# Optimization experiments

Hardware: AMD Instinct MI355X
Metric: run time of the kernel (lower is better)

The kernel has to match this reference:

```python
import jax, jax.numpy as jnp
import numpy as np

N = 100000
E = 1000000
F_IN = 128
HID = 64
HEADS = 4
NC = 4


def setup_inputs() -> dict:
    key = jax.random.key(0)
    ks = jax.random.split(key, 24)
    s = 0.05
    inp = {
        "x": jax.random.normal(ks[0], (N, F_IN), jnp.float32),
        "edge_index": jax.random.randint(ks[1], (2, E), 0, N, jnp.int64 if jax.config.jax_enable_x64 else jnp.int32),
        "edge_weight": jax.random.uniform(ks[2], (E,), jnp.float32),
        "node_mask": jnp.ones((N,), jnp.bool_),
        # GCNConv: lin (no bias applied pre-propagate in math below; bias added after)
        "gcn_W": s * jax.random.normal(ks[3], (F_IN, HID), jnp.float32),
        "gcn_b": jnp.zeros((HID,), jnp.float32),
        "proj_W": s * jax.random.normal(ks[4], (F_IN, HID), jnp.float32),
        "proj_b": jnp.zeros((HID,), jnp.float32),
        "ln1_g": jnp.ones((HID,), jnp.float32), "ln1_b": jnp.zeros((HID,), jnp.float32),
        # GATv2Conv heads=4, concat=False: lin_l, lin_r -> [F, H*C], att [H, C], bias [C]
        "gat_Wl": s * jax.random.normal(ks[5], (HID, HEADS * HID), jnp.float32),
        "gat_Wr": s * jax.random.normal(ks[6], (HID, HEADS * HID), jnp.float32),
        "gat_att": s * jax.random.normal(ks[7], (HEADS, HID), jnp.float32),
        "gat_b": jnp.zeros((HID,), jnp.float32),
        "ln2_g": jnp.ones((HID,), jnp.float32), "ln2_b": jnp.zeros((HID,), jnp.float32),
        # SAGEConv: lin_l (neighbors, with bias), lin_r (root, no bias)
        "sage_Wl": s * jax.random.normal(ks[8], (HID, HID), jnp.float32),
        "sage_bl": jnp.zeros((HID,), jnp.float32),
        "sage_Wr": s * jax.random.normal(ks[9], (HID, HID), jnp.float32),
        "ln3_g": jnp.ones((HID,), jnp.float32), "ln3_b": jnp.zeros((HID,), jnp.float32),
        # edge MLP: Linear(2*HID+1, 32) -> ReLU -> Linear(32, 1)
        "emlp_W1": s * jax.random.normal(ks[10], (2 * HID + 1, 32), jnp.float32),
        "emlp_b1": jnp.zeros((32,), jnp.float32),
        "emlp_W2": s * jax.random.normal(ks[11], (32, 1), jnp.float32),
        "emlp_b2": jnp.zeros((1,), jnp.float32),
        # heads on JK-cat dim 3*HID
        "mort_W": s * jax.random.normal(ks[12], (3 * HID, 1), jnp.float32),
        "mort_b": jnp.zeros((1,), jnp.float32),
        "hours_W": s * jax.random.normal(ks[13], (3 * HID, 1), jnp.float32),
        "hours_b": jnp.zeros((1,), jnp.float32),
        "disc_W": s * jax.random.normal(ks[14], (3 * HID, NC), jnp.float32),
        "disc_b": jnp.zeros((NC,), jnp.float32),
    }
    return inp


def _ln(h, g, b, eps=1e-5):
    mu = jnp.mean(h, axis=-1, keepdims=True)
    var = jnp.mean(jnp.square(h - mu), axis=-1, keepdims=True)
    return (h - mu) * jax.lax.rsqrt(var + eps) * g + b


def reference(x, edge_index, edge_weight, node_mask,
              gcn_W, gcn_b, proj_W, proj_b, ln1_g, ln1_b,
              gat_Wl, gat_Wr, gat_att, gat_b, ln2_g, ln2_b,
              sage_Wl, sage_bl, sage_Wr, ln3_g, ln3_b,
              emlp_W1, emlp_b1, emlp_W2, emlp_b2,
              mort_W, mort_b, hours_W, hours_b, disc_W, disc_b):
    n = x.shape[0]
    src, dst = edge_index[0], edge_index[1]
    loop = jnp.arange(n, dtype=src.dtype)
    s2 = jnp.concatenate([src, loop])  # edges + self loops (GCN, GATv2)
    d2 = jnp.concatenate([dst, loop])

    # ---- GCNConv (normalized, self loops with weight 1) ----
    w2 = jnp.concatenate([edge_weight, jnp.ones((n,), x.dtype)])
    deg = jax.ops.segment_sum(w2, d2, num_segments=n)
    dinv = jnp.where(deg > 0, jax.lax.rsqrt(deg), 0.0)
    norm = dinv[s2] * w2 * dinv[d2]
    xw = x @ gcn_W  # [N, HID]
    gcn_out = jax.ops.segment_sum(norm[:, None] * xw[s2], d2, num_segments=n) + gcn_b
    h1 = jax.nn.relu(_ln(gcn_out, ln1_g, ln1_b))
    h_init = h1 + (x @ proj_W + proj_b)

    # ---- edge-gated edge MLP (recomputed weights; unused by later convs, kept for fidelity) ----
    feat = jnp.concatenate([h_init[src], h_init[dst], edge_weight[:, None]], axis=1)
    _new_ew = jax.nn.sigmoid((jax.nn.relu(feat @ emlp_W1 + emlp_b1) @ emlp_W2 + emlp_b2)[:, 0])

    # ---- GATv2Conv (heads=4, concat=False -> mean over heads, self loops) ----
    H, C = gat_att.shape
    xl = (h_init @ gat_Wl).reshape(n, H, C)
    xr = (h_init @ gat_Wr).reshape(n, H, C)
    e = jax.nn.leaky_relu(xl[s2] + xr[d2], 0.2)        # [E+N, H, C]
    score = jnp.einsum('ehc,hc->eh', e, gat_att)        # [E+N, H]
    smax = jax.ops.segment_max(score, d2, num_segments=n)
    ex = jnp.exp(score - smax[d2])
    den = jax.ops.segment_sum(ex, d2, num_segments=n)
    alpha = ex / den[d2]
    gat_out = jax.ops.segment_sum(alpha[:, :, None] * xl[s2], d2, num_segments=n)
    gat_out = jnp.mean(gat_out, axis=1) + gat_b
    h2 = jax.nn.relu(_ln(gat_out, ln2_g, ln2_b)) + h_init

    # ---- SAGEConv (mean aggregation, root weight, no self loops) ----
    nsum = jax.ops.segment_sum(h2[src], dst, num_segments=n)
    cnt = jax.ops.segment_sum(jnp.ones(src.shape, h2.dtype), dst, num_segments=n)
    nmean = nsum / jnp.maximum(cnt, 1.0)[:, None]
    sage_out = nmean @ sage_Wl + sage_bl + h2 @ sage_Wr
    h3 = jax.nn.relu(_ln(sage_out, ln3_g, ln3_b)) + h2

    # ---- JumpingKnowledge cat + masked readout + heads ----
    x_jk = jnp.concatenate([h_init, h2, h3], axis=1)  # [N, 3*HID]
    readout = jnp.where(node_mask[:, None], x_jk, 0.0)
    mort = (readout @ mort_W + mort_b)[:, 0]
    hours = (readout @ hours_W + hours_b)[:, 0]
    disc = readout @ disc_W + disc_b
    return mort, hours, disc
```

## Files before the change

kernel.cpp:

```cpp
#include <hip/hip_runtime.h>
#include <hip/hip_fp16.h>
#include <math.h>

#define N_NODES 100000
#define N_EDGES 1000000
#define F_IN    128
#define HID     64
#define HEADS   4
#define NCLS    4
#define SCAN_BLK 98
#define GEMM_NT 5

typedef _Float16 half8 __attribute__((ext_vector_type(8)));
typedef _Float16 fp16x2 __attribute__((ext_vector_type(2)));
typedef float f32x4 __attribute__((ext_vector_type(4)));

__device__ __forceinline__ float wsum(float v) {
#pragma unroll
  for (int o = 32; o > 0; o >>= 1) v += __shfl_xor(v, o, 64);
  return v;
}
struct Half4 { __half2 a, b; };
__device__ __forceinline__ __half2 absh2(__half2 v) {
  unsigned u; __builtin_memcpy(&u, &v, 4);
  u &= 0x7FFF7FFFu;
  __half2 r; __builtin_memcpy(&r, &u, 4);
  return r;
}
__device__ __forceinline__ float fdot2f(__half2 a, __half2 b, float c) {
#if defined(__has_builtin) && __has_builtin(__builtin_amdgcn_fdot2)
  fp16x2 av, bv;
  __builtin_memcpy(&av, &a, 4); __builtin_memcpy(&bv, &b, 4);
  return __builtin_amdgcn_fdot2(av, bv, c, false);
#else
  float2 af = __half22float2(a), bf = __half22float2(b);
  return c + af.x * bf.x + af.y * bf.y;
#endif
}
__device__ __forceinline__ float edge_score(Half4 A, __half2 Ra, __half2 Rb,
                                            __half2 at0, __half2 at1,
                                            __half2 c06, __half2 c04) {
  __half2 t0 = __hadd2(A.a, Ra), t1 = __hadd2(A.b, Rb);
  __half2 l0 = __hfma2(t0, c06, __hmul2(absh2(t0), c04));
  __half2 l1 = __hfma2(t1, c06, __hmul2(absh2(t1), c04));
  return fdot2f(l1, at1, fdot2f(l0, at0, 0.f));
}
__device__ __forceinline__ float reduce16(float q) {
  q += __shfl_xor(q, 1); q += __shfl_xor(q, 2);
  q += __shfl_xor(q, 4); q += __shfl_xor(q, 8);
  return q;
}
__device__ __forceinline__ int wave_node() {
  return __builtin_amdgcn_readfirstlane(blockIdx.x * 4 + (threadIdx.x >> 6));
}

__global__ void k_hist(const int* __restrict__ dst, int* __restrict__ cnt) {
  int e = blockIdx.x * 256 + threadIdx.x;
  if (e < N_EDGES) atomicAdd(&cnt[dst[e]], 1);
}
__global__ __launch_bounds__(256) void k_scan1(const int* __restrict__ cnt,
                                               int* __restrict__ partial,
                                               int* __restrict__ bsum) {
  __shared__ int lds[256];
  int t = threadIdx.x;
  int base = blockIdx.x * 1024 + t * 4;
  int v0 = (base + 0 < N_NODES) ? cnt[base + 0] : 0;
  int v1 = (base + 1 < N_NODES) ? cnt[base + 1] : 0;
  int v2 = (base + 2 < N_NODES) ? cnt[base + 2] : 0;
  int v3 = (base + 3 < N_NODES) ? cnt[base + 3] : 0;
  int s = v0 + v1 + v2 + v3;
  lds[t] = s;
  __syncthreads();
  for (int o = 1; o < 256; o <<= 1) {
    int x = (t >= o) ? lds[t - o] : 0;
    __syncthreads();
    lds[t] += x;
    __syncthreads();
  }
  int excl = lds[t] - s;
  if (base + 0 < N_NODES) partial[base + 0] = excl;
  if (base + 1 < N_NODES) partial[base + 1] = excl + v0;
  if (base + 2 < N_NODES) partial[base + 2] = excl + v0 + v1;
  if (base + 3 < N_NODES) partial[base + 3] = excl + v0 + v1 + v2;
  if (t == 255) bsum[blockIdx.x] = lds[255];
}
__global__ __launch_bounds__(256) void k_scan3(const int* __restrict__ partial,
                                               const int* __restrict__ bsum,
                                               int* __restrict__ row_ptr,
                                               int* __restrict__ cursor) {
  __shared__ int ex[128];
  int t = threadIdx.x;
  int orig = 0;
  if (t < 128) {
    orig = (t < SCAN_BLK) ? bsum[t] : 0;
    ex[t] = orig;
  }
  __syncthreads();
  for (int o = 1; o < 128; o <<= 1) {
    int x = (t < 128 && t >= o) ? ex[t - o] : 0;
    __syncthreads();
    if (t < 128) ex[t] += x;
    __syncthreads();
  }
  if (t < 128) ex[t] -= orig;
  __syncthreads();
  int i = blockIdx.x * 256 + t;
  if (i < N_NODES) {
    int v = partial[i] + ex[i >> 10];
    row_ptr[i] = v;
    cursor[i] = v;
  }
  if (i == 0) row_ptr[N_NODES] = N_EDGES;
}
__global__ void k_fill(const int* __restrict__ src, const int* __restrict__ dst,
                       const float* __restrict__ ew, int* __restrict__ cursor,
                       int* __restrict__ csr_src, float* __restrict__ csr_w) {
  int e = blockIdx.x * 256 + threadIdx.x;
  if (e >= N_EDGES) return;
  int d = dst[e];
  int p = atomicAdd(&cursor[d], 1);
  csr_src[p] = src[e];
  csr_w[p] = ew[e];
}

__global__ __launch_bounds__(512) void k_in_gemm_mfma(
    const float* __restrict__ x, const float* __restrict__ gcn_W,
    const float* __restrict__ proj_W, const float* __restrict__ proj_b,
    __half* __restrict__ xw16, __half* __restrict__ xp16) {
  __shared__ __half at[16 * 136];
  int t = threadIdx.x;
  int w = t >> 6, lane = t & 63;
  int m = lane & 15, q = lane >> 4;
  int ncol = w * 16 + m;
  const float* W = (ncol < 64) ? gcn_W : proj_W;
  int nc = (ncol < 64) ? ncol : ncol - 64;
  half8 bf[4];
#pragma unroll
  for (int ch = 0; ch < 4; ++ch) {
    int kb = ch * 32 + q * 8;
#pragma unroll
    for (int j = 0; j < 8; ++j)
      bf[ch][j] = (_Float16)W[(kb + j) * 64 + nc];
  }
  float pb = (ncol >= 64) ? proj_b[nc] : 0.f;
  int nb0 = blockIdx.x * (16 * GEMM_NT);
  for (int nt = 0; nt < GEMM_NT; ++nt) {
    int nb = nb0 + nt * 16;
    {
      int row = t >> 5, col = (t & 31) * 4;
      float4 v = *reinterpret_cast<const float4*>(x + (size_t)(nb + row) * F_IN + col);
      __half2* d = reinterpret_cast<__half2*>(&at[row * 136 + col]);
      d[0] = __floats2half2_rn(v.x, v.y);
      d[1] = __floats2half2_rn(v.z, v.w);
    }
    __syncthreads();
    f32x4 acc = {0.f, 0.f, 0.f, 0.f};
#pragma unroll
    for (int ch = 0; ch < 4; ++ch) {
      half8 af = *reinterpret_cast<const half8*>(&at[m * 136 + ch * 32 + q * 8]);
      acc = __builtin_amdgcn_mfma_f32_16x16x32_f16(af, bf[ch], acc, 0, 0, 0);
    }
    if (ncol < 64) {
#pragma unroll
      for (int r = 0; r < 4; ++r)
        xw16[(size_t)(nb + q * 4 + r) * HID + nc] = __float2half(acc[r]);
    } else {
#pragma unroll
      for (int r = 0; r < 4; ++r)
        xp16[(size_t)(nb + q * 4 + r) * HID + nc] = __float2half(acc[r] + pb);
    }
    __syncthreads();
  }
}

__global__ void k_deg(const int* __restrict__ row_ptr, const float* __restrict__ csr_w,
                      float* __restrict__ dinv) {
  int n = blockIdx.x * 256 + threadIdx.x;
  if (n >= N_NODES) return;
  float deg = 1.0f;
  int end = row_ptr[n + 1];
  for (int i = row_ptr[n]; i < end; ++i) deg += csr_w[i];
  dinv[n] = rsqrtf(deg);
}

__global__ __launch_bounds__(256) void k_gcn_fused(
    const int* __restrict__ row_ptr, const int* __restrict__ csr_src,
    const float* __restrict__ csr_w, const float* __restrict__ dinv,
    const __half* __restrict__ xw16, const __half* __restrict__ xp16,
    const float* __restrict__ gcn_b, const float* __restrict__ g,
    const float* __restrict__ bb, __half* __restrict__ h_init16) {
  int n = wave_node();
  int lane = threadIdx.x & 63;
  float di = dinv[n];
  float acc = di * di * __half2float(xw16[(size_t)n * HID + lane]);
  int beg = row_ptr[n], end = row_ptr[n + 1];
  int i = beg;
  for (; i + 4 <= end; i += 4) {
    int s0 = __builtin_amdgcn_readfirstlane(csr_src[i]);
    int s1 = __builtin_amdgcn_readfirstlane(csr_src[i + 1]);
    int s2 = __builtin_amdgcn_readfirstlane(csr_src[i + 2]);
    int s3 = __builtin_amdgcn_readfirstlane(csr_src[i + 3]);
    float nrm0 = dinv[s0] * csr_w[i] * di;
    float nrm1 = dinv[s1] * csr_w[i + 1] * di;
    float nrm2 = dinv[s2] * csr_w[i + 2] * di;
    float nrm3 = dinv[s3] * csr_w[i + 3] * di;
    float v0 = __half2float(xw16[(size_t)s0 * HID + lane]);
    float v1 = __half2float(xw16[(size_t)s1 * HID + lane]);
    float v2 = __half2float(xw16[(size_t)s2 * HID + lane]);
    float v3 = __half2float(xw16[(size_t)s3 * HID + lane]);
    acc += nrm0 * v0 + nrm1 * v1 + nrm2 * v2 + nrm3 * v3;
  }
  for (; i < end; ++i) {
    int s = __builtin_amdgcn_readfirstlane(csr_src[i]);
    float nrm = dinv[s] * csr_w[i] * di;
    acc += nrm * __half2float(xw16[(size_t)s * HID + lane]);
  }
  float v = acc + gcn_b[lane];
  float mu = wsum(v) * (1.f / HID);
  float dv = v - mu;
  float var = wsum(dv * dv) * (1.f / HID);
  float h = dv * rsqrtf(var + 1e-5f) * g[lane] + bb[lane];
  h = h > 0.f ? h : 0.f;
  h_init16[(size_t)n * HID + lane] =
      __float2half(h + __half2float(xp16[(size_t)n * HID + lane]));
}

__global__ __launch_bounds__(512) void k_gat_gemm_mfma(
    const __half* __restrict__ h16, const float* __restrict__ Wl,
    const float* __restrict__ Wr, __half* __restrict__ xl, __half* __restrict__ xr) {
  __shared__ __half at[16 * 72];
  int t = threadIdx.x;
  int w = t >> 6, lane = t & 63;
  int m = lane & 15, q = lane >> 4;
  half8 bf[4][2];
#pragma unroll
  for (int tt = 0; tt < 4; ++tt) {
    int c = w * 16 + tt * 128 + m;
    const float* W = (c < 256) ? Wl : Wr;
    int nc = (c < 256) ? c : c - 256;
#pragma unroll
    for (int ch = 0; ch < 2; ++ch) {
      int kb = ch * 32 + q * 8;
#pragma unroll
      for (int j = 0; j < 8; ++j)
        bf[tt][ch][j] = (_Float16)W[(kb + j) * 256 + nc];
    }
  }
  int nb0 = blockIdx.x * (16 * GEMM_NT);
  for (int nt = 0; nt < GEMM_NT; ++nt) {
    int nb = nb0 + nt * 16;
    {
      int row = t >> 5, col = (t & 31) * 2;
      *reinterpret_cast<__half2*>(&at[row * 72 + col]) =
          *reinterpret_cast<const __half2*>(h16 + (size_t)(nb + row) * HID + col);
    }
    __syncthreads();
    half8 a0 = *reinterpret_cast<const half8*>(&at[m * 72 + q * 8]);
    half8 a1 = *reinterpret_cast<const half8*>(&at[m * 72 + 32 + q * 8]);
#pragma unroll
    for (int tt = 0; tt < 4; ++tt) {
      f32x4 acc = {0.f, 0.f, 0.f, 0.f};
      acc = __builtin_amdgcn_mfma_f32_16x16x32_f16(a0, bf[tt][0], acc, 0, 0, 0);
      acc = __builtin_amdgcn_mfma_f32_16x16x32_f16(a1, bf[tt][1], acc, 0, 0, 0);
      int c = w * 16 + tt * 128 + m;
      __half* out = (c < 256) ? (xl + c) : (xr + (c - 256));
#pragma unroll
      for (int r = 0; r < 4; ++r)
        out[(size_t)(nb + q * 4 + r) * 256] = __float2half(acc[r]);
    }
    __syncthreads();
  }
}

__global__ __launch_bounds__(256) void k_gat_fused(
    const int* __restrict__ row_ptr, const int* __restrict__ csr_src,
    const __half* __restrict__ xl, const __half* __restrict__ xr,
    const float* __restrict__ att, const float* __restrict__ gat_b,
    const float* __restrict__ g, const float* __restrict__ bb,
    const __half* __restrict__ h_init16, __half* __restrict__ h2_16) {
  int n = wave_node();
  int lane = threadIdx.x & 63;
  const __half2 c06 = __float2half2_rn(0.6f);
  const __half2 c04 = __float2half2_rn(0.4f);
  float4 atv = *reinterpret_cast<const float4*>(att + lane * 4);
  __half2 at0 = __floats2half2_rn(atv.x, atv.y);
  __half2 at1 = __floats2half2_rn(atv.z, atv.w);
  Half4 R = *reinterpret_cast<const Half4*>(xr + (size_t)n * 256 + lane * 4);
  Half4 S = *reinterpret_cast<const Half4*>(xl + (size_t)n * 256 + lane * 4);

  float q = reduce16(edge_score(S, R.a, R.b, at0, at1, c06, c04));
  float w = __expf(q);
  float den = w;
  float2 f0 = __half22float2(S.a), f1 = __half22float2(S.b);
  float4 acc = make_float4(w * f0.x, w * f0.y, w * f1.x, w * f1.y);

  int beg = row_ptr[n], end = row_ptr[n + 1];
  int i = beg;
  for (; i + 4 <= end; i += 4) {
    int s0 = __builtin_amdgcn_readfirstlane(csr_src[i]);
    int s1 = __builtin_amdgcn_readfirstlane(csr_src[i + 1]);
    int s2 = __builtin_amdgcn_readfirstlane(csr_src[i + 2]);
    int s3 = __builtin_amdgcn_readfirstlane(csr_src[i + 3]);
    Half4 A0 = *reinterpret_cast<const Half4*>(xl + (size_t)s0 * 256 + lane * 4);
    Half4 A1 = *reinterpret_cast<const Half4*>(xl + (size_t)s1 * 256 + lane * 4);
    Half4 A2 = *reinterpret_cast<const Half4*>(xl + (size_t)s2 * 256 + lane * 4);
    Half4 A3 = *reinterpret_cast<const Half4*>(xl + (size_t)s3 * 256 + lane * 4);
    float q0 = edge_score(A0, R.a, R.b, at0, at1, c06, c04);
    float q1 = edge_score(A1, R.a, R.b, at0, at1, c06, c04);
    float q2 = edge_score(A2, R.a, R.b, at0, at1, c06, c04);
    float q3 = edge_score(A3, R.a, R.b, at0, at1, c06, c04);
    q0 += __shfl_xor(q0, 1); q1 += __shfl_xor(q1, 1);
    q2 += __shfl_xor(q2, 1); q3 += __shfl_xor(q3, 1);
    q0 += __shfl_xor(q0, 2); q1 += __shfl_xor(q1, 2);
    q2 += __shfl_xor(q2, 2); q3 += __shfl_xor(q3, 2);
    q0 += __shfl_xor(q0, 4); q1 += __shfl_xor(q1, 4);
    q2 += __shfl_xor(q2, 4); q3 += __shfl_xor(q3, 4);
    q0 += __shfl_xor(q0, 8); q1 += __shfl_xor(q1, 8);
    q2 += __shfl_xor(q2, 8); q3 += __shfl_xor(q3, 8);
    float w0 = __expf(q0), w1 = __expf(q1);
    float w2 = __expf(q2), w3 = __expf(q3);
    den += (w0 + w1) + (w2 + w3);
    float2 a00 = __half22float2(A0.a), a01 = __half22float2(A0.b);
    float2 a10 = __half22float2(A1.a), a11 = __half22float2(A1.b);
    float2 a20 = __half22float2(A2.a), a21 = __half22float2(A2.b);
    float2 a30 = __half22float2(A3.a), a31 = __half22float2(A3.b);
    acc.x += (w0 * a00.x + w1 * a10.x) + (w2 * a20.x + w3 * a30.x);
    acc.y += (w0 * a00.y + w1 * a10.y) + (w2 * a20.y + w3 * a30.y);
    acc.z += (w0 * a01.x + w1 * a11.x) + (w2 * a21.x + w3 * a31.x);
    acc.w += (w0 * a01.y + w1 * a11.y) + (w2 * a21.y + w3 * a31.y);
  }
  for (; i < end; ++i) {
    int s0 = __builtin_amdgcn_readfirstlane(csr_src[i]);
    Half4 A0 = *reinterpret_cast<const Half4*>(xl + (size_t)s0 * 256 + lane * 4);
    q = reduce16(edge_score(A0, R.a, R.b, at0, at1, c06, c04));
    w = __expf(q);
    den += w;
    float2 a00 = __half22float2(A0.a), a01 = __half22float2(A0.b);
    acc.x += w * a00.x; acc.y += w * a00.y;
    acc.z += w * a01.x; acc.w += w * a01.y;
  }
  float inv = 1.f / den;
  acc.x *= inv; acc.y *= inv; acc.z *= inv; acc.w *= inv;
  acc.x += __shfl_xor(acc.x, 16); acc.y += __shfl_xor(acc.y, 16);
  acc.z += __shfl_xor(acc.z, 16); acc.w += __shfl_xor(acc.w, 16);
  acc.x += __shfl_xor(acc.x, 32); acc.y += __shfl_xor(acc.y, 32);
  acc.z += __shfl_xor(acc.z, 32); acc.w += __shfl_xor(acc.w, 32);
  int srcl = lane >> 2;
  float t0 = __shfl(acc.x, srcl), t1 = __shfl(acc.y, srcl);
  float t2 = __shfl(acc.z, srcl), t3 = __shfl(acc.w, srcl);
  int r = lane & 3;
  float mean = (r == 0) ? t0 : (r == 1) ? t1 : (r == 2) ? t2 : t3;
  float val = mean * 0.25f + gat_b[lane];
  float mu = wsum(val) * (1.f / HID);
  float dv = val - mu;
  float var = wsum(dv * dv) * (1.f / HID);
  float h = dv * rsqrtf(var + 1e-5f) * g[lane] + bb[lane];
  h = h > 0.f ? h : 0.f;
  float outv = h + __half2float(h_init16[(size_t)n * HID + lane]);
  h2_16[(size_t)n * HID + lane] = __float2half(outv);
}

__global__ __launch_bounds__(256) void k_sage_gather(
    const int* __restrict__ row_ptr, const int* __restrict__ csr_src,
    const __half* __restrict__ h2_16, __half* __restrict__ nmean16) {
  int n = wave_node();
  int lane = threadIdx.x & 63;
  int beg = row_ptr[n], end = row_ptr[n + 1];
  float sum = 0.f;
  int i = beg;
  for (; i + 4 <= end; i += 4) {
    int s0 = __builtin_amdgcn_readfirstlane(csr_src[i]);
    int s1 = __builtin_amdgcn_readfirstlane(csr_src[i + 1]);
    int s2 = __builtin_amdgcn_readfirstlane(csr_src[i + 2]);
    int s3 = __builtin_amdgcn_readfirstlane(csr_src[i + 3]);
    float v0 = __half2float(h2_16[(size_t)s0 * HID + lane]);
    float v1 = __half2float(h2_16[(size_t)s1 * HID + lane]);
    float v2 = __half2float(h2_16[(size_t)s2 * HID + lane]);
    float v3 = __half2float(h2_16[(size_t)s3 * HID + lane]);
    sum += v0 + v1 + v2 + v3;
  }
  for (; i < end; ++i) {
    int s = __builtin_amdgcn_readfirstlane(csr_src[i]);
    sum += __half2float(h2_16[(size_t)s * HID + lane]);
  }
  nmean16[(size_t)n * HID + lane] =
      __float2half(sum / fmaxf((float)(end - beg), 1.f));
}

__global__ __launch_bounds__(64) void k_sage_gemm_ln_heads(
    const __half* __restrict__ nmean16, const __half* __restrict__ h2_16,
    const __half* __restrict__ h_init16,
    const float* __restrict__ Wl, const float* __restrict__ Wr,
    const float* __restrict__ sage_bl, const float* __restrict__ g,
    const float* __restrict__ bb, const int* __restrict__ mask,
    const float* __restrict__ mort_W, const float* __restrict__ mort_b,
    const float* __restrict__ hours_W, const float* __restrict__ hours_b,
    const float* __restrict__ disc_W, const float* __restrict__ disc_b,
    float* __restrict__ out) {
  __shared__ float nt[8][HID];
  __shared__ float ht[8][HID];
  int t = threadIdx.x;
  int n0 = blockIdx.x * 8;
  {
    const __half* np = nmean16 + (size_t)n0 * HID + t * 8;
    const __half* hp = h2_16 + (size_t)n0 * HID + t * 8;
    Half4 n0v = *reinterpret_cast<const Half4*>(np);
    Half4 n1v = *reinterpret_cast<const Half4*>(np + 4);
    Half4 p0 = *reinterpret_cast<const Half4*>(hp);
    Half4 p1 = *reinterpret_cast<const Half4*>(hp + 4);
    float* dn = &nt[0][0] + t * 8;
    float* dh = &ht[0][0] + t * 8;
    float2 f;
    f = __half22float2(n0v.a); dn[0] = f.x; dn[1] = f.y;
    f = __half22float2(n0v.b); dn[2] = f.x; dn[3] = f.y;
    f = __half22float2(n1v.a); dn[4] = f.x; dn[5] = f.y;
    f = __half22float2(n1v.b); dn[6] = f.x; dn[7] = f.y;
    f = __half22float2(p0.a);  dh[0] = f.x; dh[1] = f.y;
    f = __half22float2(p0.b);  dh[2] = f.x; dh[3] = f.y;
    f = __half22float2(p1.a);  dh[4] = f.x; dh[5] = f.y;
    f = __half22float2(p1.b);  dh[6] = f.x; dh[7] = f.y;
  }
  __syncthreads();
  int f = t;
  float acc[8] = {0.f,0.f,0.f,0.f,0.f,0.f,0.f,0.f};
  for (int k = 0; k < HID; k += 4) {
    float wl0 = Wl[(k + 0) * HID + f], wr0 = Wr[(k + 0) * HID + f];
    float wl1 = Wl[(k + 1) * HID + f], wr1 = Wr[(k + 1) * HID + f];
    float wl2 = Wl[(k + 2) * HID + f], wr2 = Wr[(k + 2) * HID + f];
    float wl3 = Wl[(k + 3) * HID + f], wr3 = Wr[(k + 3) * HID + f];
#pragma unroll
    for (int j = 0; j < 8; ++j) {
      float4 nv = *reinterpret_cast<const float4*>(&nt[j][k]);
      float4 hv = *reinterpret_cast<const float4*>(&ht[j][k]);
      acc[j] += nv.x * wl0 + nv.y * wl1 + nv.z * wl2 + nv.w * wl3
              + hv.x * wr0 + hv.y * wr1 + hv.z * wr2 + hv.w * wr3;
    }
  }
  float blv = sage_bl[f], gv = g[f], bbv = bb[f];
  float mw0 = mort_W[f], mw1 = mort_W[64 + f], mw2 = mort_W[128 + f];
// ... 43 lines not shown
  const float* x       = (const float*)d_in[0];
  const int*   ei      = (const int*)d_in[1];
  const float* ew      = (const float*)d_in[2];
  const int*   mask    = (const int*)d_in[3];
  const float* gcn_W   = (const float*)d_in[4];
  const float* gcn_b   = (const float*)d_in[5];
  const float* proj_W  = (const float*)d_in[6];
  const float* proj_b  = (const float*)d_in[7];
  const float* ln1_g   = (const float*)d_in[8];
  const float* ln1_b   = (const float*)d_in[9];
  const float* gat_Wl  = (const float*)d_in[10];
  const float* gat_Wr  = (const float*)d_in[11];
  const float* gat_att = (const float*)d_in[12];
  const float* gat_b   = (const float*)d_in[13];
  const float* ln2_g   = (const float*)d_in[14];
  const float* ln2_b   = (const float*)d_in[15];
  const float* sage_Wl = (const float*)d_in[16];
  const float* sage_bl = (const float*)d_in[17];
  const float* sage_Wr = (const float*)d_in[18];
  const float* ln3_g   = (const float*)d_in[19];
  const float* ln3_b   = (const float*)d_in[20];
  const float* mort_W  = (const float*)d_in[25];
  const float* mort_b  = (const float*)d_in[26];
  const float* hours_W = (const float*)d_in[27];
  const float* hours_b = (const float*)d_in[28];
  const float* disc_W  = (const float*)d_in[29];
  const float* disc_b  = (const float*)d_in[30];

  const int* src = ei;
  const int* dst = ei + N_EDGES;
  float* out = (float*)d_out;

  float* ws = (float*)d_ws;
  const size_t F = (size_t)N_NODES * HID;
  __half* xp16  = (__half*)(ws + 2 * F);
  __half* xl    = (__half*)(ws + 3 * F);
  __half* xw16  = xl;
  __half* nmean16 = (__half*)(ws + 3 * F);
  __half* xr    = (__half*)(ws + 3 * F + (size_t)N_NODES * 128);
  __half* h2_16 = (__half*)(ws + 3 * F + (size_t)N_NODES * 256);
  __half* h_init16 = (__half*)(ws + 3 * F + (size_t)N_NODES * 288);
  float* tail   = ws + 3 * F + (size_t)N_NODES * 320;
  int*   csr_src = (int*)tail;           tail += N_EDGES;
  float* csr_w   = tail;                 tail += N_EDGES;
  int*   row_ptr = (int*)tail;           tail += N_NODES + 64;
  int*   cursor  = (int*)tail;           tail += N_NODES;
  int*   cnt     = (int*)tail;           tail += N_NODES;
  int*   partial = (int*)tail;           tail += N_NODES;
  int*   bsum    = (int*)tail;           tail += 128;
  float* dinv    = tail;

  const int GE = (N_EDGES + 255) / 256;
  const int GN = (N_NODES + 255) / 256;
  const int GB = N_NODES / (16 * GEMM_NT);

  hipMemsetAsync(cnt, 0, N_NODES * sizeof(int), stream);
  k_hist<<<GE, 256, 0, stream>>>(dst, cnt);
  k_scan1<<<SCAN_BLK, 256, 0, stream>>>(cnt, partial, bsum);
  k_scan3<<<GN, 256, 0, stream>>>(partial, bsum, row_ptr, cursor);
  k_fill<<<GE, 256, 0, stream>>>(src, dst, ew, cursor, csr_src, csr_w);

  k_in_gemm_mfma<<<GB, 512, 0, stream>>>(x, gcn_W, proj_W, proj_b, xw16, xp16);
  k_deg<<<GN, 256, 0, stream>>>(row_ptr, csr_w, dinv);
  k_gcn_fused<<<N_NODES / 4, 256, 0, stream>>>(row_ptr, csr_src, csr_w, dinv, xw16,
                                               xp16, gcn_b, ln1_g, ln1_b, h_init16);

  k_gat_gemm_mfma<<<GB, 512, 0, stream>>>(h_init16, gat_Wl, gat_Wr, xl, xr);
  k_gat_fused<<<N_NODES / 4, 256, 0, stream>>>(row_ptr, csr_src, xl, xr, gat_att,
                                               gat_b, ln2_g, ln2_b, h_init16, h2_16);

  k_sage_gather<<<N_NODES / 4, 256, 0, stream>>>(row_ptr, csr_src, h2_16, nmean16);
  k_sage_gemm_ln_heads<<<N_NODES / 8, 64, 0, stream>>>(
      nmean16, h2_16, h_init16, sage_Wl, sage_Wr, sage_bl, ln3_g, ln3_b, mask,
      mort_W, mort_b, hours_W, hours_b, disc_W, disc_b, out);
}
```

Measured before the change: 562.3 us.

## Fuse histogram and degree into input GEMM; restructure GAT gather per half-wave

The edge histogram and weighted-degree accumulation now run as extra blocks of the input GEMM launch, using float atomics into the cursor buffer. dinv is computed in the scan kernel, which removes the separate k_deg pass over the CSR. The GAT aggregation kernel is rewritten so each half-wave handles one edge with 8 halves per lane, giving two edges in flight per iteration and wider 16-byte loads. The LayerNorm epilogue is vectorised to match. This trades float atomic contention and a changed summation order against fewer launches and better memory-level parallelism.

```diff
diff --git a/kernel.cpp b/kernel.cpp
--- a/kernel.cpp
+++ b/kernel.cpp
@@ -10,6 +10,8 @@
 #define NCLS    4
 #define SCAN_BLK 98
 #define GEMM_NT 5
+#define GB_GEMM (N_NODES / (16 * GEMM_NT))
+#define GH_HIST ((N_EDGES + 511) / 512)
 
 typedef _Float16 half8 __attribute__((ext_vector_type(8)));
 typedef _Float16 fp16x2 __attribute__((ext_vector_type(2)));
@@ -37,13 +39,30 @@
   return c + af.x * bf.x + af.y * bf.y;
 #endif
 }
-__device__ __forceinline__ float edge_score(Half4 A, __half2 Ra, __half2 Rb,
-                                            __half2 at0, __half2 at1,
-                                            __half2 c06, __half2 c04) {
-  __half2 t0 = __hadd2(A.a, Ra), t1 = __hadd2(A.b, Rb);
-  __half2 l0 = __hfma2(t0, c06, __hmul2(absh2(t0), c04));
-  __half2 l1 = __hfma2(t1, c06, __hmul2(absh2(t1), c04));
-  return fdot2f(l1, at1, fdot2f(l0, at0, 0.f));
+__device__ __forceinline__ __half2 h2of(half8 v, int p) {
+  fp16x2 t; t[0] = v[2 * p]; t[1] = v[2 * p + 1];
+  __half2 r; __builtin_memcpy(&r, &t, 4);
+  return r;
+}
+__device__ __forceinline__ float score8(half8 A, half8 R,
+                                        __half2 at0, __half2 at1,
+                                        __half2 at2, __half2 at3,
+                                        __half2 c06, __half2 c04) {
+  __half2 t, l;
+  float q = 0.f;
+  t = __hadd2(h2of(A, 0), h2of(R, 0));
+  l = __hfma2(t, c06, __hmul2(absh2(t), c04));
+  q = fdot2f(l, at0, q);
+  t = __hadd2(h2of(A, 1), h2of(R, 1));
+  l = __hfma2(t, c06, __hmul2(absh2(t), c04));
+  q = fdot2f(l, at1, q);
+  t = __hadd2(h2of(A, 2), h2of(R, 2));
+  l = __hfma2(t, c06, __hmul2(absh2(t), c04));
+  q = fdot2f(l, at2, q);
+  t = __hadd2(h2of(A, 3), h2of(R, 3));
+  l = __hfma2(t, c06, __hmul2(absh2(t), c04));
+  q = fdot2f(l, at3, q);
+  return q;
 }
 __device__ __forceinline__ float reduce16(float q) {
   q += __shfl_xor(q, 1); q += __shfl_xor(q, 2);
@@ -54,10 +73,6 @@
   return __builtin_amdgcn_readfirstlane(blockIdx.x * 4 + (threadIdx.x >> 6));
 }
 
-__global__ void k_hist(const int* __restrict__ dst, int* __restrict__ cnt) {
-  int e = blockIdx.x * 256 + threadIdx.x;
-  if (e < N_EDGES) atomicAdd(&cnt[dst[e]], 1);
-}
 __global__ __launch_bounds__(256) void k_scan1(const int* __restrict__ cnt,
                                                int* __restrict__ partial,
                                                int* __restrict__ bsum) {
@@ -87,7 +102,8 @@
 __global__ __launch_bounds__(256) void k_scan3(const int* __restrict__ partial,
                                                const int* __restrict__ bsum,
                                                int* __restrict__ row_ptr,
-                                               int* __restrict__ cursor) {
+                                               int* __restrict__ cursor,
+                                               float* __restrict__ dinv) {
   __shared__ int ex[128];
   int t = threadIdx.x;
   int orig = 0;
@@ -106,6 +122,8 @@
   __syncthreads();
   int i = blockIdx.x * 256 + t;
   if (i < N_NODES) {
+    int raw = cursor[i];
+    dinv[i] = rsqrtf(1.0f + __int_as_float(raw));
     int v = partial[i] + ex[i >> 10];
     row_ptr[i] = v;
     cursor[i] = v;
@@ -123,11 +141,22 @@
   csr_w[p] = ew[e];
 }
 
-__global__ __launch_bounds__(512) void k_in_gemm_mfma(
+__global__ __launch_bounds__(512) void k_in_gemm_hist(
     const float* __restrict__ x, const float* __restrict__ gcn_W,
     const float* __restrict__ proj_W, const float* __restrict__ proj_b,
-    __half* __restrict__ xw16, __half* __restrict__ xp16) {
+    __half* __restrict__ xw16, __half* __restrict__ xp16,
+    const int* __restrict__ dst, const float* __restrict__ ew,
+    int* __restrict__ cnt, float* __restrict__ degf) {
   __shared__ __half at[16 * 136];
+  if (blockIdx.x >= GB_GEMM) {
+    int e = (blockIdx.x - GB_GEMM) * 512 + threadIdx.x;
+    if (e < N_EDGES) {
+      int d = dst[e];
+      atomicAdd(&cnt[d], 1);
+      atomicAdd(&degf[d], ew[e]);
+    }
+    return;
+  }
   int t = threadIdx.x;
   int w = t >> 6, lane = t & 63;
   int m = lane & 15, q = lane >> 4;
@@ -171,16 +200,6 @@
     }
     __syncthreads();
   }
-}
-
-__global__ void k_deg(const int* __restrict__ row_ptr, const float* __restrict__ csr_w,
-                      float* __restrict__ dinv) {
-  int n = blockIdx.x * 256 + threadIdx.x;
-  if (n >= N_NODES) return;
-  float deg = 1.0f;
-  int end = row_ptr[n + 1];
-  for (int i = row_ptr[n]; i < end; ++i) deg += csr_w[i];
-  dinv[n] = rsqrtf(deg);
 }
 
 __global__ __launch_bounds__(256) void k_gcn_fused(
@@ -276,88 +295,123 @@
     const int* __restrict__ row_ptr, const int* __restrict__ csr_src,
     const __half* __restrict__ xl, const __half* __restrict__ xr,
     const float* __restrict__ att, const float* __restrict__ gat_b,
-    const float* __restrict__ g, const float* __restrict__ bb,
+    const float* __restrict__ lng, const float* __restrict__ lnb,
     const __half* __restrict__ h_init16, __half* __restrict__ h2_16) {
   int n = wave_node();
   int lane = threadIdx.x & 63;
+  int H = lane >> 5;
+  int l32 = lane & 31;
+  int oc = l32 & 7;
   const __half2 c06 = __float2half2_rn(0.6f);
   const __half2 c04 = __float2half2_rn(0.4f);
-  float4 atv = *reinterpret_cast<const float4*>(att + lane * 4);
-  __half2 at0 = __floats2half2_rn(atv.x, atv.y);
-  __half2 at1 = __floats2half2_rn(atv.z, atv.w);
-  Half4 R = *reinterpret_cast<const Half4*>(xr + (size_t)n * 256 + lane * 4);
-  Half4 S = *reinterpret_cast<const Half4*>(xl + (size_t)n * 256 + lane * 4);
-
-  float q = reduce16(edge_score(S, R.a, R.b, at0, at1, c06, c04));
-  float w = __expf(q);
-  float den = w;
-  float2 f0 = __half22float2(S.a), f1 = __half22float2(S.b);
-  float4 acc = make_float4(w * f0.x, w * f0.y, w * f1.x, w * f1.y);
-
+  float4 a0 = *reinterpret_cast<const float4*>(att + l32 * 8);
+  float4 a1 = *reinterpret_cast<const float4*>(att + l32 * 8 + 4);
+  __half2 at0 = __floats2half2_rn(a0.x, a0.y), at1 = __floats2half2_rn(a0.z, a0.w);
+  __half2 at2 = __floats2half2_rn(a1.x, a1.y), at3 = __floats2half2_rn(a1.z, a1.w);
+  const __half* xlb = xl + l32 * 8;
+  half8 R = *reinterpret_cast<const half8*>(xr + (size_t)n * 256 + l32 * 8);
+  half8 S = *reinterpret_cast<const half8*>(xl + (size_t)n * 256 + l32 * 8);
+
+  float acc[8];
+  float den;
+  {
+    float q = score8(S, R, at0, at1, at2, at3, c06, c04);
+    q += __shfl_xor(q, 1); q += __shfl_xor(q, 2); q += __shfl_xor(q, 4);
+    float w = (H == 0) ? __expf(q) : 0.f;
+    den = w;
+#pragma unroll
+    for (int j = 0; j < 8; ++j) acc[j] = w * (float)S[j];
+  }
   int beg = row_ptr[n], end = row_ptr[n + 1];
   int i = beg;
-  for (; i + 4 <= end; i += 4) {
-    int s0 = __builtin_amdgcn_readfirstlane(csr_src[i]);
-    int s1 = __builtin_amdgcn_readfirstlane(csr_src[i + 1]);
-    int s2 = __builtin_amdgcn_readfirstlane(csr_src[i + 2]);
-    int s3 = __builtin_amdgcn_readfirstlane(csr_src[i + 3]);
-    Half4 A0 = *reinterpret_cast<const Half4*>(xl + (size_t)s0 * 256 + lane * 4);
-    Half4 A1 = *reinterpret_cast<const Half4*>(xl + (size_t)s1 * 256 + lane * 4);
-    Half4 A2 = *reinterpret_cast<const Half4*>(xl + (size_t)s2 * 256 + lane * 4);
-    Half4 A3 = *reinterpret_cast<const Half4*>(xl + (size_t)s3 * 256 + lane * 4);
-    float q0 = edge_score(A0, R.a, R.b, at0, at1, c06, c04);
-    float q1 = edge_score(A1, R.a, R.b, at0, at1, c06, c04);
-    float q2 = edge_score(A2, R.a, R.b, at0, at1, c06, c04);
-    float q3 = edge_score(A3, R.a, R.b, at0, at1, c06, c04);
+  for (; i + 8 <= end; i += 8) {
+    int s0 = csr_src[i + 0 + H];
+    int s1 = csr_src[i + 2 + H];
+    int s2 = csr_src[i + 4 + H];
+    int s3 = csr_src[i + 6 + H];
+    half8 A0 = *reinterpret_cast<const half8*>(xlb + (unsigned)s0 * 256u);
+    half8 A1 = *reinterpret_cast<const half8*>(xlb + (unsigned)s1 * 256u);
+    half8 A2 = *reinterpret_cast<const half8*>(xlb + (unsigned)s2 * 256u);
+    half8 A3 = *reinterpret_cast<const half8*>(xlb + (unsigned)s3 * 256u);
+    float q0 = score8(A0, R, at0, at1, at2, at3, c06, c04);
+    float q1 = score8(A1, R, at0, at1, at2, at3, c06, c04);
+    float q2 = score8(A2, R, at0, at1, at2, at3, c06, c04);
+    float q3 = score8(A3, R, at0, at1, at2, at3, c06, c04);
     q0 += __shfl_xor(q0, 1); q1 += __shfl_xor(q1, 1);
     q2 += __shfl_xor(q2, 1); q3 += __shfl_xor(q3, 1);
     q0 += __shfl_xor(q0, 2); q1 += __shfl_xor(q1, 2);
     q2 += __shfl_xor(q2, 2); q3 += __shfl_xor(q3, 2);
     q0 += __shfl_xor(q0, 4); q1 += __shfl_xor(q1, 4);
     q2 += __shfl_xor(q2, 4); q3 += __shfl_xor(q3, 4);
-    q0 += __shfl_xor(q0, 8); q1 += __shfl_xor(q1, 8);
-    q2 += __shfl_xor(q2, 8); q3 += __shfl_xor(q3, 8);
-    float w0 = __expf(q0), w1 = __expf(q1);
-    float w2 = __expf(q2), w3 = __expf(q3);
+    float w0 = __expf(q0), w1 = __expf(q1), w2 = __expf(q2), w3 = __expf(q3);
     den += (w0 + w1) + (w2 + w3);
-    float2 a00 = __half22float2(A0.a), a01 = __half22float2(A0.b);
-    float2 a10 = __half22float2(A1.a), a11 = __half22float2(A1.b);
-    float2 a20 = __half22float2(A2.a), a21 = __half22float2(A2.b);
-    float2 a30 = __half22float2(A3.a), a31 = __half22float2(A3.b);
-    acc.x += (w0 * a00.x + w1 * a10.x) + (w2 * a20.x + w3 * a30.x);
-    acc.y += (w0 * a00.y + w1 * a10.y) + (w2 * a20.y + w3 * a30.y);
-    acc.z += (w0 * a01.x + w1 * a11.x) + (w2 * a21.x + w3 * a31.x);
-    acc.w += (w0 * a01.y + w1 * a11.y) + (w2 * a21.y + w3 * a31.y);
-  }
-  for (; i < end; ++i) {
-    int s0 = __builtin_amdgcn_readfirstlane(csr_src[i]);
-    Half4 A0 = *reinterpret_cast<const Half4*>(xl + (size_t)s0 * 256 + lane * 4);
-    q = reduce16(edge_score(A0, R.a, R.b, at0, at1, c06, c04));
-    w = __expf(q);
+#pragma unroll
+    for (int j = 0; j < 8; ++j) {
+      float a = fmaf(w0, (float)A0[j], acc[j]);
+      a = fmaf(w1, (float)A1[j], a);
+      a = fmaf(w2, (float)A2[j], a);
+      acc[j] = fmaf(w3, (float)A3[j], a);
+    }
+  }
+  for (; i < end; i += 2) {
+    int e = i + H;
+    bool valid = e < end;
+    int ec = valid ? e : i;
+    int s0 = csr_src[ec];
+    half8 A0 = *reinterpret_cast<const half8*>(xlb + (unsigned)s0 * 256u);
+    float q = score8(A0, R, at0, at1, at2, at3, c06, c04);
+    q += __shfl_xor(q, 1); q += __shfl_xor(q, 2); q += __shfl_xor(q, 4);
+    float w = valid ? __expf(q) : 0.f;
     den += w;
-    float2 a00 = __half22float2(A0.a), a01 = __half22float2(A0.b);
-    acc.x += w * a00.x; acc.y += w * a00.y;
-    acc.z += w * a01.x; acc.w += w * a01.y;
-  }
+#pragma unroll
+    for (int j = 0; j < 8; ++j) acc[j] = fmaf(w, (float)A0[j], acc[j]);
+  }
+  den += __shfl_xor(den, 32);
+#pragma unroll
+  for (int j = 0; j < 8; ++j) acc[j] += __shfl_xor(acc[j], 32);
   float inv = 1.f / den;
-  acc.x *= inv; acc.y *= inv; acc.z *= inv; acc.w *= inv;
-  acc.x += __shfl_xor(acc.x, 16); acc.y += __shfl_xor(acc.y, 16);
-  acc.z += __shfl_xor(acc.z, 16); acc.w += __shfl_xor(acc.w, 16);
-  acc.x += __shfl_xor(acc.x, 32); acc.y += __shfl_xor(acc.y, 32);
-  acc.z += __shfl_xor(acc.z, 32); acc.w += __shfl_xor(acc.w, 32);
-  int srcl = lane >> 2;
-  float t0 = __shfl(acc.x, srcl), t1 = __shfl(acc.y, srcl);
-  float t2 = __shfl(acc.z, srcl), t3 = __shfl(acc.w, srcl);
-  int r = lane & 3;
-  float mean = (r == 0) ? t0 : (r == 1) ? t1 : (r == 2) ? t2 : t3;
-  float val = mean * 0.25f + gat_b[lane];
-  float mu = wsum(val) * (1.f / HID);
-  float dv = val - mu;
-  float var = wsum(dv * dv) * (1.f / HID);
-  float h = dv * rsqrtf(var + 1e-5f) * g[lane] + bb[lane];
-  h = h > 0.f ? h : 0.f;
-  float outv = h + __half2float(h_init16[(size_t)n * HID + lane]);
-  h2_16[(size_t)n * HID + lane] = __float2half(outv);
+#pragma unroll
+  for (int j = 0; j < 8; ++j) acc[j] *= inv;
+#pragma unroll
+  for (int j = 0; j < 8; ++j) acc[j] += __shfl_xor(acc[j], 8);
+#pragma unroll
+  for (int j = 0; j < 8; ++j) acc[j] += __shfl_xor(acc[j], 16);
+  float4 gb0 = *reinterpret_cast<const float4*>(gat_b + oc * 8);
+  float4 gb1 = *reinterpret_cast<const float4*>(gat_b + oc * 8 + 4);
+  float vals[8];
+  vals[0] = fmaf(acc[0], 0.25f, gb0.x);
+  vals[1] = fmaf(acc[1], 0.25f, gb0.y);
+  vals[2] = fmaf(acc[2], 0.25f, gb0.z);
+  vals[3] = fmaf(acc[3], 0.25f, gb0.w);
+  vals[4] = fmaf(acc[4], 0.25f, gb1.x);
+  vals[5] = fmaf(acc[5], 0.25f, gb1.y);
+  vals[6] = fmaf(acc[6], 0.25f, gb1.z);
+  vals[7] = fmaf(acc[7], 0.25f, gb1.w);
+  float s8 = ((vals[0] + vals[1]) + (vals[2] + vals[3])) +
+             ((vals[4] + vals[5]) + (vals[6] + vals[7]));
+  s8 += __shfl_xor(s8, 1); s8 += __shfl_xor(s8, 2); s8 += __shfl_xor(s8, 4);
+  float mu = s8 * (1.f / HID);
+  float dv[8]; float v8 = 0.f;
+#pragma unroll
+  for (int j = 0; j < 8; ++j) { dv[j] = vals[j] - mu; v8 = fmaf(dv[j], dv[j], v8); }
+  v8 += __shfl_xor(v8, 1); v8 += __shfl_xor(v8, 2); v8 += __shfl_xor(v8, 4);
+  float rstd = rsqrtf(v8 * (1.f / HID) + 1e-5f);
+  float4 g0 = *reinterpret_cast<const float4*>(lng + oc * 8);
+  float4 g1 = *reinterpret_cast<const float4*>(lng + oc * 8 + 4);
+  float4 b0 = *reinterpret_cast<const float4*>(lnb + oc * 8);
+  float4 b1 = *reinterpret_cast<const float4*>(lnb + oc * 8 + 4);
+  float gg[8]  = {g0.x, g0.y, g0.z, g0.w, g1.x, g1.y, g1.z, g1.w};
+  float bbv[8] = {b0.x, b0.y, b0.z, b0.w, b1.x, b1.y, b1.z, b1.w};
+  half8 hi = *reinterpret_cast<const half8*>(h_init16 + (size_t)n * HID + oc * 8);
+  half8 outv;
+#pragma unroll
+  for (int j = 0; j < 8; ++j) {
+    float h = fmaf(dv[j] * rstd, gg[j], bbv[j]);
+    h = h > 0.f ? h : 0.f;
+    outv[j] = (_Float16)(h + (float)hi[j]);
+  }
+  if (lane < 8)
+    *reinterpret_cast<half8*>(h2_16 + (size_t)n * HID + lane * 8) = outv;
 }
 
 __global__ __launch_bounds__(256) void k_sage_gather(
@@ -534,20 +588,18 @@
 
   const int GE = (N_EDGES + 255) / 256;
   const int GN = (N_NODES + 255) / 256;
-  const int GB = N_NODES / (16 * GEMM_NT);
-
-  hipMemsetAsync(cnt, 0, N_NODES * sizeof(int), stream);
-  k_hist<<<GE, 256, 0, stream>>>(dst, cnt);
+
+  hipMemsetAsync(cursor, 0, 2 * N_NODES * sizeof(int), stream);
+  k_in_gemm_hist<<<GB_GEMM + GH_HIST, 512, 0, stream>>>(
+      x, gcn_W, proj_W, proj_b, xw16, xp16, dst, ew, cnt, (float*)cursor);
   k_scan1<<<SCAN_BLK, 256, 0, stream>>>(cnt, partial, bsum);
-  k_scan3<<<GN, 256, 0, stream>>>(partial, bsum, row_ptr, cursor);
+  k_scan3<<<GN, 256, 0, stream>>>(partial, bsum, row_ptr, cursor, dinv);
   k_fill<<<GE, 256, 0, stream>>>(src, dst, ew, cursor, csr_src, csr_w);
 
-  k_in_gemm_mfma<<<GB, 512, 0, stream>>>(x, gcn_W, proj_W, proj_b, xw16, xp16);
-  k_deg<<<GN, 256, 0, stream>>>(row_ptr, csr_w, dinv);
   k_gcn_fused<<<N_NODES / 4, 256, 0, stream>>>(row_ptr, csr_src, csr_w, dinv, xw16,
                                                xp16, gcn_b, ln1_g, ln1_b, h_init16);
 
-  k_gat_gemm_mfma<<<GB, 512, 0, stream>>>(h_init16, gat_Wl, gat_Wr, xl, xr);
+  k_gat_gemm_mfma<<<GB_GEMM, 512, 0, stream>>>(h_init16, gat_Wl, gat_Wr, xl, xr);
   k_gat_fused<<<N_NODES / 4, 256, 0, stream>>>(row_ptr, csr_src, xl, xr, gat_att,
                                                gat_b, ln2_g, ln2_b, h_init16, h2_16);
 
```

New measurement: 606.5 us. 7.9% more time.

## Gather four neighbor rows per wave with 16-lane groups in GCN and SAGE

Applied to the files above, without the earlier changes.

The GCN and SAGE gather kernels now split each wave into four 16-lane groups. Each group loads one neighbor's 64-half row as 8-byte vectors, so four edges are processed per iteration instead of one edge per 2-byte lane load. Partial sums are combined with cross-group shuffles, and the GCN LayerNorm is reworked for four values per lane. The GAT kernel switches from the Half4 struct to a native half4 vector type with explicit fmaf accumulation. Tail edges are masked rather than branched, which wastes some lanes on low-degree nodes, and the row offset now uses 32-bit indexing.

```diff
diff --git a/kernel.cpp b/kernel.cpp
--- a/kernel.cpp
+++ b/kernel.cpp
@@ -12,6 +12,7 @@
 #define GEMM_NT 5
 
 typedef _Float16 half8 __attribute__((ext_vector_type(8)));
+typedef _Float16 half4v __attribute__((ext_vector_type(4)));
 typedef _Float16 fp16x2 __attribute__((ext_vector_type(2)));
 typedef float f32x4 __attribute__((ext_vector_type(4)));
 
@@ -37,10 +38,16 @@
   return c + af.x * bf.x + af.y * bf.y;
 #endif
 }
-__device__ __forceinline__ float edge_score(Half4 A, __half2 Ra, __half2 Rb,
+__device__ __forceinline__ __half2 h2of4(half4v v, int p) {
+  fp16x2 t; t[0] = v[2 * p]; t[1] = v[2 * p + 1];
+  __half2 r; __builtin_memcpy(&r, &t, 4);
+  return r;
+}
+__device__ __forceinline__ float edge_score(half4v A, half4v R,
                                             __half2 at0, __half2 at1,
                                             __half2 c06, __half2 c04) {
-  __half2 t0 = __hadd2(A.a, Ra), t1 = __hadd2(A.b, Rb);
+  __half2 t0 = __hadd2(h2of4(A, 0), h2of4(R, 0));
+  __half2 t1 = __hadd2(h2of4(A, 1), h2of4(R, 1));
   __half2 l0 = __hfma2(t0, c06, __hmul2(absh2(t0), c04));
   __half2 l1 = __hfma2(t1, c06, __hmul2(absh2(t1), c04));
   return fdot2f(l1, at1, fdot2f(l0, at0, 0.f));
@@ -191,38 +198,58 @@
     const float* __restrict__ bb, __half* __restrict__ h_init16) {
   int n = wave_node();
   int lane = threadIdx.x & 63;
+  int grp = lane >> 4;
+  int c = lane & 15;
   float di = dinv[n];
-  float acc = di * di * __half2float(xw16[(size_t)n * HID + lane]);
+  half4v sv = *reinterpret_cast<const half4v*>(xw16 + (size_t)n * HID + c * 4);
+  float sl = (grp == 0) ? di * di : 0.f;
+  float a0 = sl * (float)sv[0];
+  float a1 = sl * (float)sv[1];
+  float a2 = sl * (float)sv[2];
+  float a3 = sl * (float)sv[3];
   int beg = row_ptr[n], end = row_ptr[n + 1];
-  int i = beg;
-  for (; i + 4 <= end; i += 4) {
-    int s0 = __builtin_amdgcn_readfirstlane(csr_src[i]);
-    int s1 = __builtin_amdgcn_readfirstlane(csr_src[i + 1]);
-    int s2 = __builtin_amdgcn_readfirstlane(csr_src[i + 2]);
-    int s3 = __builtin_amdgcn_readfirstlane(csr_src[i + 3]);
-    float nrm0 = dinv[s0] * csr_w[i] * di;
-    float nrm1 = dinv[s1] * csr_w[i + 1] * di;
-    float nrm2 = dinv[s2] * csr_w[i + 2] * di;
-    float nrm3 = dinv[s3] * csr_w[i + 3] * di;
-    float v0 = __half2float(xw16[(size_t)s0 * HID + lane]);
-    float v1 = __half2float(xw16[(size_t)s1 * HID + lane]);
-    float v2 = __half2float(xw16[(size_t)s2 * HID + lane]);
-    float v3 = __half2float(xw16[(size_t)s3 * HID + lane]);
-    acc += nrm0 * v0 + nrm1 * v1 + nrm2 * v2 + nrm3 * v3;
-  }
-  for (; i < end; ++i) {
-    int s = __builtin_amdgcn_readfirstlane(csr_src[i]);
-    float nrm = dinv[s] * csr_w[i] * di;
-    acc += nrm * __half2float(xw16[(size_t)s * HID + lane]);
-  }
-  float v = acc + gcn_b[lane];
-  float mu = wsum(v) * (1.f / HID);
-  float dv = v - mu;
-  float var = wsum(dv * dv) * (1.f / HID);
-  float h = dv * rsqrtf(var + 1e-5f) * g[lane] + bb[lane];
-  h = h > 0.f ? h : 0.f;
-  h_init16[(size_t)n * HID + lane] =
-      __float2half(h + __half2float(xp16[(size_t)n * HID + lane]));
+  for (int i = beg; i < end; i += 4) {
+    int e = i + grp;
+    bool valid = e < end;
+    int ec = valid ? e : beg;
+    int sidx = csr_src[ec];
+    float wv = csr_w[ec];
+    float dv = dinv[sidx];
+    float nrm = valid ? dv * wv * di : 0.f;
+    half4v r = *reinterpret_cast<const half4v*>(
+        xw16 + (unsigned)((unsigned)sidx * HID + c * 4));
+    a0 = fmaf(nrm, (float)r[0], a0);
+    a1 = fmaf(nrm, (float)r[1], a1);
+    a2 = fmaf(nrm, (float)r[2], a2);
+    a3 = fmaf(nrm, (float)r[3], a3);
+  }
+  a0 += __shfl_xor(a0, 16); a1 += __shfl_xor(a1, 16);
+  a2 += __shfl_xor(a2, 16); a3 += __shfl_xor(a3, 16);
+  a0 += __shfl_xor(a0, 32); a1 += __shfl_xor(a1, 32);
+  a2 += __shfl_xor(a2, 32); a3 += __shfl_xor(a3, 32);
+  float4 gb = *reinterpret_cast<const float4*>(gcn_b + c * 4);
+  float v0 = a0 + gb.x, v1 = a1 + gb.y, v2 = a2 + gb.z, v3 = a3 + gb.w;
+  float s = (v0 + v1) + (v2 + v3);
+  s += __shfl_xor(s, 1); s += __shfl_xor(s, 2);
+  s += __shfl_xor(s, 4); s += __shfl_xor(s, 8);
+  float mu = s * (1.f / HID);
+  float d0 = v0 - mu, d1 = v1 - mu, d2 = v2 - mu, d3 = v3 - mu;
+  float qq = fmaf(d0, d0, fmaf(d1, d1, fmaf(d2, d2, d3 * d3)));
+  qq += __shfl_xor(qq, 1); qq += __shfl_xor(qq, 2);
+  qq += __shfl_xor(qq, 4); qq += __shfl_xor(qq, 8);
+  float rstd = rsqrtf(qq * (1.f / HID) + 1e-5f);
+  float4 gv = *reinterpret_cast<const float4*>(g + c * 4);
+  float4 bv = *reinterpret_cast<const float4*>(bb + c * 4);
+  half4v px = *reinterpret_cast<const half4v*>(xp16 + (size_t)n * HID + c * 4);
+  if (grp == 0) {
+    half4v o;
+    float h;
+    h = fmaf(d0 * rstd, gv.x, bv.x); h = h > 0.f ? h : 0.f; o[0] = (_Float16)(h + (float)px[0]);
+    h = fmaf(d1 * rstd, gv.y, bv.y); h = h > 0.f ? h : 0.f; o[1] = (_Float16)(h + (float)px[1]);
+    h = fmaf(d2 * rstd, gv.z, bv.z); h = h > 0.f ? h : 0.f; o[2] = (_Float16)(h + (float)px[2]);
+    h = fmaf(d3 * rstd, gv.w, bv.w); h = h > 0.f ? h : 0.f; o[3] = (_Float16)(h + (float)px[3]);
+    *reinterpret_cast<half4v*>(h_init16 + (size_t)n * HID + c * 4) = o;
+  }
 }
 
 __global__ __launch_bounds__(512) void k_gat_gemm_mfma(
@@ -285,14 +312,14 @@
   float4 atv = *reinterpret_cast<const float4*>(att + lane * 4);
   __half2 at0 = __floats2half2_rn(atv.x, atv.y);
   __half2 at1 = __floats2half2_rn(atv.z, atv.w);
-  Half4 R = *reinterpret_cast<const Half4*>(xr + (size_t)n * 256 + lane * 4);
-  Half4 S = *reinterpret_cast<const Half4*>(xl + (size_t)n * 256 + lane * 4);
-
-  float q = reduce16(edge_score(S, R.a, R.b, at0, at1, c06, c04));
+  half4v R = *reinterpret_cast<const half4v*>(xr + (size_t)n * 256 + lane * 4);
+  half4v S = *reinterpret_cast<const half4v*>(xl + (size_t)n * 256 + lane * 4);
+
+  float q = reduce16(edge_score(S, R, at0, at1, c06, c04));
   float w = __expf(q);
   float den = w;
-  float2 f0 = __half22float2(S.a), f1 = __half22float2(S.b);
-  float4 acc = make_float4(w * f0.x, w * f0.y, w * f1.x, w * f1.y);
+  float ax = w * (float)S[0], ay = w * (float)S[1];
+  float az = w * (float)S[2], aw = w * (float)S[3];
 
   int beg = row_ptr[n], end = row_ptr[n + 1];
   int i = beg;
@@ -301,14 +328,14 @@
     int s1 = __builtin_amdgcn_readfirstlane(csr_src[i + 1]);
     int s2 = __builtin_amdgcn_readfirstlane(csr_src[i + 2]);
     int s3 = __builtin_amdgcn_readfirstlane(csr_src[i + 3]);
-    Half4 A0 = *reinterpret_cast<const Half4*>(xl + (size_t)s0 * 256 + lane * 4);
-    Half4 A1 = *reinterpret_cast<const Half4*>(xl + (size_t)s1 * 256 + lane * 4);
-    Half4 A2 = *reinterpret_cast<const Half4*>(xl + (size_t)s2 * 256 + lane * 4);
-    Half4 A3 = *reinterpret_cast<const Half4*>(xl + (size_t)s3 * 256 + lane * 4);
-    float q0 = edge_score(A0, R.a, R.b, at0, at1, c06, c04);
-    float q1 = edge_score(A1, R.a, R.b, at0, at1, c06, c04);
-    float q2 = edge_score(A2, R.a, R.b, at0, at1, c06, c04);
-    float q3 = edge_score(A3, R.a, R.b, at0, at1, c06, c04);
+    half4v A0 = *reinterpret_cast<const half4v*>(xl + (size_t)s0 * 256 + lane * 4);
+    half4v A1 = *reinterpret_cast<const half4v*>(xl + (size_t)s1 * 256 + lane * 4);
+    half4v A2 = *reinterpret_cast<const half4v*>(xl + (size_t)s2 * 256 + lane * 4);
+    half4v A3 = *reinterpret_cast<const half4v*>(xl + (size_t)s3 * 256 + lane * 4);
+    float q0 = edge_score(A0, R, at0, at1, c06, c04);
+    float q1 = edge_score(A1, R, at0, at1, c06, c04);
+    float q2 = edge_score(A2, R, at0, at1, c06, c04);
+    float q3 = edge_score(A3, R, at0, at1, c06, c04);
     q0 += __shfl_xor(q0, 1); q1 += __shfl_xor(q1, 1);
     q2 += __shfl_xor(q2, 1); q3 += __shfl_xor(q3, 1);
     q0 += __shfl_xor(q0, 2); q1 += __shfl_xor(q1, 2);
@@ -320,34 +347,33 @@
     float w0 = __expf(q0), w1 = __expf(q1);
     float w2 = __expf(q2), w3 = __expf(q3);
     den += (w0 + w1) + (w2 + w3);
-    float2 a00 = __half22float2(A0.a), a01 = __half22float2(A0.b);
-    float2 a10 = __half22float2(A1.a), a11 = __half22float2(A1.b);
-    float2 a20 = __half22float2(A2.a), a21 = __half22float2(A2.b);
-    float2 a30 = __half22float2(A3.a), a31 = __half22float2(A3.b);
-    acc.x += (w0 * a00.x + w1 * a10.x) + (w2 * a20.x + w3 * a30.x);
-    acc.y += (w0 * a00.y + w1 * a10.y) + (w2 * a20.y + w3 * a30.y);
-    acc.z += (w0 * a01.x + w1 * a11.x) + (w2 * a21.x + w3 * a31.x);
-    acc.w += (w0 * a01.y + w1 * a11.y) + (w2 * a21.y + w3 * a31.y);
+    ax = fmaf(w0, (float)A0[0], ax); ax = fmaf(w1, (float)A1[0], ax);
+    ax = fmaf(w2, (float)A2[0], ax); ax = fmaf(w3, (float)A3[0], ax);
+    ay = fmaf(w0, (float)A0[1], ay); ay = fmaf(w1, (float)A1[1], ay);
+    ay = fmaf(w2, (float)A2[1], ay); ay = fmaf(w3, (float)A3[1], ay);
+    az = fmaf(w0, (float)A0[2], az); az = fmaf(w1, (float)A1[2], az);
+    az = fmaf(w2, (float)A2[2], az); az = fmaf(w3, (float)A3[2], az);
+    aw = fmaf(w0, (float)A0[3], aw); aw = fmaf(w1, (float)A1[3], aw);
+    aw = fmaf(w2, (float)A2[3], aw); aw = fmaf(w3, (float)A3[3], aw);
   }
   for (; i < end; ++i) {
     int s0 = __builtin_amdgcn_readfirstlane(csr_src[i]);
-    Half4 A0 = *reinterpret_cast<const Half4*>(xl + (size_t)s0 * 256 + lane * 4);
-    q = reduce16(edge_score(A0, R.a, R.b, at0, at1, c06, c04));
+    half4v A0 = *reinterpret_cast<const half4v*>(xl + (size_t)s0 * 256 + lane * 4);
+    q = reduce16(edge_score(A0, R, at0, at1, c06, c04));
     w = __expf(q);
     den += w;
-    float2 a00 = __half22float2(A0.a), a01 = __half22float2(A0.b);
-    acc.x += w * a00.x; acc.y += w * a00.y;
-    acc.z += w * a01.x; acc.w += w * a01.y;
+    ax = fmaf(w, (float)A0[0], ax); ay = fmaf(w, (float)A0[1], ay);
+    az = fmaf(w, (float)A0[2], az); aw = fmaf(w, (float)A0[3], aw);
   }
   float inv = 1.f / den;
-  acc.x *= inv; acc.y *= inv; acc.z *= inv; acc.w *= inv;
-  acc.x += __shfl_xor(acc.x, 16); acc.y += __shfl_xor(acc.y, 16);
-  acc.z += __shfl_xor(acc.z, 16); acc.w += __shfl_xor(acc.w, 16);
-  acc.x += __shfl_xor(acc.x, 32); acc.y += __shfl_xor(acc.y, 32);
-  acc.z += __shfl_xor(acc.z, 32); acc.w += __shfl_xor(acc.w, 32);
+  ax *= inv; ay *= inv; az *= inv; aw *= inv;
+  ax += __shfl_xor(ax, 16); ay += __shfl_xor(ay, 16);
+  az += __shfl_xor(az, 16); aw += __shfl_xor(aw, 16);
+  ax += __shfl_xor(ax, 32); ay += __shfl_xor(ay, 32);
+  az += __shfl_xor(az, 32); aw += __shfl_xor(aw, 32);
   int srcl = lane >> 2;
-  float t0 = __shfl(acc.x, srcl), t1 = __shfl(acc.y, srcl);
-  float t2 = __shfl(acc.z, srcl), t3 = __shfl(acc.w, srcl);
+  float t0 = __shfl(ax, srcl), t1 = __shfl(ay, srcl);
+  float t2 = __shfl(az, srcl), t3 = __shfl(aw, srcl);
   int r = lane & 3;
   float mean = (r == 0) ? t0 : (r == 1) ? t1 : (r == 2) ? t2 : t3;
   float val = mean * 0.25f + gat_b[lane];
@@ -365,26 +391,36 @@
     const __half* __restrict__ h2_16, __half* __restrict__ nmean16) {
   int n = wave_node();
   int lane = threadIdx.x & 63;
+  int grp = lane >> 4;
+  int c = lane & 15;
   int beg = row_ptr[n], end = row_ptr[n + 1];
-  float sum = 0.f;
-  int i = beg;
-  for (; i + 4 <= end; i += 4) {
-    int s0 = __builtin_amdgcn_readfirstlane(csr_src[i]);
-    int s1 = __builtin_amdgcn_readfirstlane(csr_src[i + 1]);
-    int s2 = __builtin_amdgcn_readfirstlane(csr_src[i + 2]);
-    int s3 = __builtin_amdgcn_readfirstlane(csr_src[i + 3]);
-    float v0 = __half2float(h2_16[(size_t)s0 * HID + lane]);
-    float v1 = __half2float(h2_16[(size_t)s1 * HID + lane]);
-    float v2 = __half2float(h2_16[(size_t)s2 * HID + lane]);
-    float v3 = __half2float(h2_16[(size_t)s3 * HID + lane]);
-    sum += v0 + v1 + v2 + v3;
-  }
-  for (; i < end; ++i) {
-    int s = __builtin_amdgcn_readfirstlane(csr_src[i]);
-    sum += __half2float(h2_16[(size_t)s * HID + lane]);
-  }
-  nmean16[(size_t)n * HID + lane] =
-      __float2half(sum / fmaxf((float)(end - beg), 1.f));
+  float a0 = 0.f, a1 = 0.f, a2 = 0.f, a3 = 0.f;
+  for (int i = beg; i < end; i += 4) {
+    int e = i + grp;
+    bool valid = e < end;
+    int ec = valid ? e : beg;
+    int sidx = csr_src[ec];
+    float m = valid ? 1.f : 0.f;
+    half4v r = *reinterpret_cast<const half4v*>(
+        h2_16 + (unsigned)((unsigned)sidx * HID + c * 4));
+    a0 = fmaf(m, (float)r[0], a0);
+    a1 = fmaf(m, (float)r[1], a1);
+    a2 = fmaf(m, (float)r[2], a2);
+    a3 = fmaf(m, (float)r[3], a3);
+  }
+  a0 += __shfl_xor(a0, 16); a1 += __shfl_xor(a1, 16);
+  a2 += __shfl_xor(a2, 16); a3 += __shfl_xor(a3, 16);
+  a0 += __shfl_xor(a0, 32); a1 += __shfl_xor(a1, 32);
+  a2 += __shfl_xor(a2, 32); a3 += __shfl_xor(a3, 32);
+  if (grp == 0) {
+    float inv = 1.f / fmaxf((float)(end - beg), 1.f);
+    half4v o;
+    o[0] = (_Float16)(a0 * inv);
+    o[1] = (_Float16)(a1 * inv);
+    o[2] = (_Float16)(a2 * inv);
+    o[3] = (_Float16)(a3 * inv);
+    *reinterpret_cast<half4v*>(nmean16 + (size_t)n * HID + c * 4) = o;
+  }
 }
 
 __global__ __launch_bounds__(64) void k_sage_gemm_ln_heads(
```

After: 580.9 us. +3.3%, slower.
